# Performance work log

Measured on AMD Instinct MI355X. Metric: run time of the kernel, lower is better.

Reference implementation:

```python
import jax, jax.numpy as jnp
import numpy as np

B, T, I, H, L = 128, 512, 512, 1024, 2
KEEP = 0.9  # 1 - dropout_rate


def setup_inputs() -> dict:
    key = jax.random.key(0)
    ks = jax.random.split(key, 13)
    s = 0.02
    bern = lambda k, shape: (jax.random.bernoulli(k, KEEP, shape) / KEEP).astype(jnp.float32)
    return {
        "x": jax.random.normal(ks[0], (B, T, I), dtype=jnp.float32),
        "W_ih0": jax.random.normal(ks[1], (4 * H, I), dtype=jnp.float32) * s,
        "W_hh0": jax.random.normal(ks[2], (4 * H, H), dtype=jnp.float32) * s,
        "b_ih0": jax.random.normal(ks[3], (4 * H,), dtype=jnp.float32) * s,
        "b_hh0": jax.random.normal(ks[4], (4 * H,), dtype=jnp.float32) * s,
        "W_ih1": jax.random.normal(ks[5], (4 * H, H), dtype=jnp.float32) * s,
        "W_hh1": jax.random.normal(ks[6], (4 * H, H), dtype=jnp.float32) * s,
        "b_ih1": jax.random.normal(ks[7], (4 * H,), dtype=jnp.float32) * s,
        "b_hh1": jax.random.normal(ks[8], (4 * H,), dtype=jnp.float32) * s,
        "out_mask": bern(ks[9], (L, B, H)),
        "h_mask": bern(ks[10], (L, B, H)),
        "c_mask": bern(ks[11], (L, B, H)),
    }


def _run_layer(x_tbi, W_ih, W_hh, b_ih, b_hh, om, hm, cm):
    """x_tbi: [T,B,in]; masks: [B,H]. Returns ([T,B,H] outputs, final (h,c))."""
    h0 = jnp.zeros((x_tbi.shape[1], H), dtype=x_tbi.dtype)
    c0 = jnp.zeros_like(h0)
    # precompute input projections for all timesteps: [T,B,4H]
    xg = jnp.einsum('tbi,gi->tbg', x_tbi, W_ih) + b_ih + b_hh

    def step(carry, xg_t):
        h, c = carry
        gates = xg_t + h @ W_hh.T  # [B,4H]
        i, f, g, o = jnp.split(gates, 4, axis=-1)
        i, f, o = jax.nn.sigmoid(i), jax.nn.sigmoid(f), jax.nn.sigmoid(o)
        g = jnp.tanh(g)
        c2 = f * c + i * g
        h2 = o * jnp.tanh(c2)
        out = h2 * om
        return (h2 * hm, c2 * cm), out

    (hf, cf), ys = jax.lax.scan(step, (h0, c0), xg)
    return ys, (hf, cf)


def reference(x, W_ih0, W_hh0, b_ih0, b_hh0, W_ih1, W_hh1, b_ih1, b_hh1,
              out_mask, h_mask, c_mask):
    layers = [(W_ih0, W_hh0, b_ih0, b_hh0), (W_ih1, W_hh1, b_ih1, b_hh1)]
    xt = jnp.transpose(x, (1, 0, 2))  # [T,B,I]
    for l, (Wi, Wh, bi, bh) in enumerate(layers):
        xt, (hf, cf) = _run_layer(xt, Wi, Wh, bi, bh,
                                  out_mask[l], h_mask[l], c_mask[l])
    out = jnp.transpose(xt, (1, 0, 2))  # [B,T,H]
    return out, (hf[None], cf[None])
```

## Files before the change

kernel.cpp:

```cpp
#include <hip/hip_runtime.h>

#define B_  128
#define T_  512
#define I_  512
#define H_  1024
#define G4  4096
#define SLOT 262144L
#define SENTW 0xFFFFFFFFu

typedef __attribute__((ext_vector_type(8))) short   short8;
typedef __attribute__((ext_vector_type(4))) short   short4v;
typedef __attribute__((ext_vector_type(4))) float   f32x4;
typedef unsigned long long u64;

__device__ __forceinline__ float bf2f(short u){
  return __uint_as_float(((unsigned)(unsigned short)u) << 16);
}
__device__ __forceinline__ short f2bf(float f){
  unsigned u = __float_as_uint(f);
  unsigned r = (u + 0x7FFFu + ((u >> 16) & 1u)) >> 16;
  return (short)r;
}
__device__ __forceinline__ float sigm(float x){ return 1.0f/(1.0f + __expf(-x)); }
__device__ __forceinline__ float tanh_(float x){ return 1.0f - 2.0f/(__expf(2.0f*x) + 1.0f); }
__device__ __forceinline__ bool okq(u64 a){
  return ((unsigned)a != SENTW) & ((unsigned)(a >> 32) != SENTW);
}

__global__ __launch_bounds__(256) void cvt_bf16(const float* __restrict__ in,
                                                short* __restrict__ out, int nq){
  int i = blockIdx.x*256 + threadIdx.x;
  if (i >= nq) return;
  float4 v = ((const float4*)in)[i];
  short4v o; o.x = f2bf(v.x); o.y = f2bf(v.y); o.z = f2bf(v.z); o.w = f2bf(v.w);
  ((short4v*)out)[i] = o;
}

__global__ __launch_bounds__(256) void swz_whh(const float* __restrict__ W,
                                               short* __restrict__ out){
  int c = blockIdx.x*256 + threadIdx.x;
  int l = c & 63, ks = (c >> 6) & 15, ct = (c >> 10) & 1, wvv = (c >> 11) & 7, jb = c >> 14;
  int g = wvv >> 1, kh = wvv & 1;
  long row = (long)(g*1024 + jb*32 + ct*16 + (l & 15));
  int col = kh*512 + ks*32 + (l >> 4)*8;
  const float* src = W + row*H_ + col;
  short8 o;
#pragma unroll
  for (int e = 0; e < 8; ++e) o[e] = f2bf(src[e]);
  ((short8*)out)[c] = o;
}

template<int K>
__global__ __launch_bounds__(256) void proj_gemm(const short* __restrict__ A,
                                                 const short* __restrict__ W,
                                                 const float* __restrict__ bih,
                                                 const float* __restrict__ bhh,
                                                 short* __restrict__ C){
  __shared__ short lds[2][2][128*40];
  const int tid = threadIdx.x;
  const int l  = tid & 63, wv = tid >> 6;
  const int wm = wv >> 1,  wn = wv & 1;
  const int nt = blockIdx.x, mt = blockIdx.y;
  const int r0 = tid >> 2, cb = (tid & 3) * 8;
  const short* Ab = A + (long)(mt*128 + r0)*K + cb;
  const short* Wb = W + (long)(nt*128 + r0)*K + cb;
  const int lo  = r0*40 + cb;
  const int lo2 = lo + 64*40;
  const int NK = K/32;

  short8 pa0 = *(const short8*)(Ab);
  short8 pa1 = *(const short8*)(Ab + 64*K);
  short8 pb0 = *(const short8*)(Wb);
  short8 pb1 = *(const short8*)(Wb + 64*K);
  *(short8*)&lds[0][0][lo]  = pa0;
  *(short8*)&lds[0][0][lo2] = pa1;
  *(short8*)&lds[0][1][lo]  = pb0;
  *(short8*)&lds[0][1][lo2] = pb1;

  f32x4 acc[4][4];
  f32x4 z = {0.f,0.f,0.f,0.f};
#pragma unroll
  for (int i = 0; i < 4; ++i)
#pragma unroll
    for (int j = 0; j < 4; ++j) acc[i][j] = z;

  for (int kt = 0; kt < NK; ++kt){
    __syncthreads();
    if (kt + 1 < NK){
      pa0 = *(const short8*)(Ab + (kt+1)*32);
      pa1 = *(const short8*)(Ab + (kt+1)*32 + 64*K);
      pb0 = *(const short8*)(Wb + (kt+1)*32);
      pb1 = *(const short8*)(Wb + (kt+1)*32 + 64*K);
    }
    const short* As = lds[kt & 1][0];
    const short* Bs = lds[kt & 1][1];
    short8 bfr[4];
#pragma unroll
    for (int nf = 0; nf < 4; ++nf)
      bfr[nf] = *(const short8*)&Bs[(wn*64 + nf*16 + (l & 15))*40 + (l >> 4)*8];
#pragma unroll
    for (int mf = 0; mf < 4; ++mf){
      short8 af = *(const short8*)&As[(wm*64 + mf*16 + (l & 15))*40 + (l >> 4)*8];
#pragma unroll
      for (int nf = 0; nf < 4; ++nf)
        acc[mf][nf] = __builtin_amdgcn_mfma_f32_16x16x32_bf16(af, bfr[nf], acc[mf][nf], 0, 0, 0);
    }
    if (kt + 1 < NK){
      int nb = (kt + 1) & 1;
      *(short8*)&lds[nb][0][lo]  = pa0;
      *(short8*)&lds[nb][0][lo2] = pa1;
      *(short8*)&lds[nb][1][lo]  = pb0;
      *(short8*)&lds[nb][1][lo2] = pb1;
    }
  }

  const int mrow0 = mt*128 + wm*64;
  const int ncol0 = nt*128 + wn*64;
#pragma unroll
  for (int nf = 0; nf < 4; ++nf){
    int n = ncol0 + nf*16 + (l & 15);
    int g   = n >> 10;
    int jb  = (n & 1023) >> 5;
    int jl5 = n & 31;
    float bs = bih[n] + bhh[n];
#pragma unroll
    for (int mf = 0; mf < 4; ++mf){
#pragma unroll
      for (int r = 0; r < 4; ++r){
        int m = mrow0 + mf*16 + (l >> 4)*4 + r;
        int b = m >> 9, t = m & 511;
        int idx2 = (jl5 >> 3)*16 + (b & 15);
        int pos  = (idx2 >> 3)*64 + (idx2 & 7)*8 + (jl5 & 7);
        long o = ((((long)t*8 + (b >> 4))*32 + jb)*4 + g)*512 + pos;
        C[o] = f2bf(acc[mf][nf][r] + bs);
      }
    }
  }
}

template<int LAYER, bool RING>
__global__ __launch_bounds__(512, 2) void lstm_scan(
    short* __restrict__ hring,
    const short* __restrict__ Wsw, const short* __restrict__ xg,
    const float* __restrict__ om, const float* __restrict__ hm, const float* __restrict__ cm,
    short* __restrict__ out0, float* __restrict__ dout,
    int* __restrict__ flags)
{
  const int tid = threadIdx.x;
  const int l = tid & 63, wv = tid >> 6;
  const int bt = blockIdx.x, jb = blockIdx.y;

  short8 w0[16], w1[16];
  {
    const short8* wp = (const short8*)Wsw + ((long)((jb*8 + wv)*2)*16)*64 + l;
#pragma unroll
    for (int ks = 0; ks < 16; ++ks) w0[ks] = wp[ks*64];
#pragma unroll
    for (int ks = 0; ks < 16; ++ks) w1[ks] = wp[(16 + ks)*64];
    f32x4* wf0 = (f32x4*)w0;
    f32x4* wf1 = (f32x4*)w1;
#pragma unroll
    for (int i = 0; i < 16; ++i){ asm volatile("" : "+v"(wf0[i])); asm volatile("" : "+v"(wf1[i])); }
  }

  const int idx = wv*8 + (l >> 3);
  const int bl  = idx & 15;
  const int jl  = ((idx >> 4) << 3) + (l & 7);
  const int jcol = jb*32 + jl;
  const long bj = (long)(bt*16 + bl)*H_ + jcol;
  const float mo = om[bj], mh = hm[bj], mc = cm[bj];
  float c = 0.f;
  const int ct_r = jl >> 4;
  const int lane_src = (jl & 15) + ((bl >> 2) << 4);
  const int rr = bl & 3;
  const int kh = wv & 1;

  __shared__ __align__(16) short hbuf[2048*8];
  __shared__ float red[16*264];
  __shared__ __align__(16) short sstage[512];
  int* flbase = flags + (long)bt*T_*32;

  const long go0 = (long)(wv*256 + 0*64 + l)*2;
  const long go1 = (long)(wv*256 + 1*64 + l)*2;
  const long go2 = (long)(wv*256 + 2*64 + l)*2;
  const long go3 = (long)(wv*256 + 3*64 + l)*2;

  const short* xg0 = xg + (((long)bt)*32 + jb)*2048;
  short xv0 = xg0[tid], xv1 = xg0[512 + tid], xv2 = xg0[1024 + tid], xv3 = xg0[1536 + tid];

  for (int t = 0; t < T_; ++t){
    const long slotoff  = RING ? (long)t*SLOT     : (long)(t & 1)*SLOT;
    const long nslotoff = RING ? (long)(t+1)*SLOT : (long)((t+1) & 1)*SLOT;

    if (t > 0){
      const u64* hp = (const u64*)((const char*)hring + slotoff + (long)bt*32768);
      if constexpr (RING){
        u64 q0=0,q1=0,q2=0,q3=0,q4=0,q5=0,q6=0,q7=0;
        int ok = 0, spins = 0;
        while (true){
          if (!(ok & 1)){
            u64 a = __hip_atomic_load(hp + go0,     __ATOMIC_RELAXED, __HIP_MEMORY_SCOPE_AGENT);
            u64 b = __hip_atomic_load(hp + go0 + 1, __ATOMIC_RELAXED, __HIP_MEMORY_SCOPE_AGENT);
            if (okq(a) & okq(b)){ q0 = a; q1 = b; ok |= 1; }
          }
          if (!(ok & 2)){
            u64 a = __hip_atomic_load(hp + go1,     __ATOMIC_RELAXED, __HIP_MEMORY_SCOPE_AGENT);
            u64 b = __hip_atomic_load(hp + go1 + 1, __ATOMIC_RELAXED, __HIP_MEMORY_SCOPE_AGENT);
            if (okq(a) & okq(b)){ q2 = a; q3 = b; ok |= 2; }
          }
          if (!(ok & 4)){
            u64 a = __hip_atomic_load(hp + go2,     __ATOMIC_RELAXED, __HIP_MEMORY_SCOPE_AGENT);
            u64 b = __hip_atomic_load(hp + go2 + 1, __ATOMIC_RELAXED, __HIP_MEMORY_SCOPE_AGENT);
            if (okq(a) & okq(b)){ q4 = a; q5 = b; ok |= 4; }
          }
          if (!(ok & 8)){
            u64 a = __hip_atomic_load(hp + go3,     __ATOMIC_RELAXED, __HIP_MEMORY_SCOPE_AGENT);
            u64 b = __hip_atomic_load(hp + go3 + 1, __ATOMIC_RELAXED, __HIP_MEMORY_SCOPE_AGENT);
            if (okq(a) & okq(b)){ q6 = a; q7 = b; ok |= 8; }
          }
          if (ok == 15) break;
          if (++spins > (1 << 20)) break;
          if (spins > 2) __builtin_amdgcn_s_sleep(2);
        }
        union { u64 u[2]; short8 s; } c0, c1, c2_, c3;
        c0.u[0] = q0; c0.u[1] = q1;  c1.u[0] = q2; c1.u[1] = q3;
        c2_.u[0] = q4; c2_.u[1] = q5; c3.u[0] = q6; c3.u[1] = q7;
        *(short8*)&hbuf[(wv*256 +   0 + l)*8] = c0.s;
        *(short8*)&hbuf[(wv*256 +  64 + l)*8] = c1.s;
        *(short8*)&hbuf[(wv*256 + 128 + l)*8] = c2_.s;
        *(short8*)&hbuf[(wv*256 + 192 + l)*8] = c3.s;
      } else {
        short8 vv[4];
#pragma unroll
        for (int i = 0; i < 4; ++i){
          const u64* ap = hp + (long)(wv*256 + i*64 + l)*2;
          union { u64 q[2]; short8 s; } uu;
          uu.q[0] = __hip_atomic_load(ap,     __ATOMIC_RELAXED, __HIP_MEMORY_SCOPE_AGENT);
          uu.q[1] = __hip_atomic_load(ap + 1, __ATOMIC_RELAXED, __HIP_MEMORY_SCOPE_AGENT);
          vv[i] = uu.s;
        }
#pragma unroll
        for (int i = 0; i < 4; ++i)
          *(short8*)&hbuf[(wv*256 + i*64 + l)*8] = vv[i];
      }
      __syncthreads();

      f32x4 a00 = {0.f,0.f,0.f,0.f}, a01 = {0.f,0.f,0.f,0.f};
      f32x4 a10 = {0.f,0.f,0.f,0.f}, a11 = {0.f,0.f,0.f,0.f};
#pragma unroll
      for (int ks = 0; ks < 16; ++ks){
        short8 av = *(const short8*)&hbuf[((kh*16 + ks)*64 + l)*8];
        if (ks & 1){
          a01 = __builtin_amdgcn_mfma_f32_16x16x32_bf16(av, w0[ks], a01, 0, 0, 0);
          a11 = __builtin_amdgcn_mfma_f32_16x16x32_bf16(av, w1[ks], a11, 0, 0, 0);
        } else {
          a00 = __builtin_amdgcn_mfma_f32_16x16x32_bf16(av, w0[ks], a00, 0, 0, 0);
          a10 = __builtin_amdgcn_mfma_f32_16x16x32_bf16(av, w1[ks], a10, 0, 0, 0);
        }
      }
      f32x4 s0, s1;
#pragma unroll
      for (int r = 0; r < 4; ++r){ s0[r] = a00[r] + a01[r]; s1[r] = a10[r] + a11[r]; }
      *(f32x4*)&red[(wv*2 + 0)*264 + l*4] = s0;
      *(f32x4*)&red[(wv*2 + 1)*264 + l*4] = s1;
      __syncthreads();
    }

    float gate[4];
    short xvv[4] = {xv0, xv1, xv2, xv3};
#pragma unroll
    for (int g = 0; g < 4; ++g){
      float rv = 0.f;
      if (t > 0){
        rv = red[((g*2 + 0)*2 + ct_r)*264 + lane_src*4 + rr]
           + red[((g*2 + 1)*2 + ct_r)*264 + lane_src*4 + rr];
      }
      gate[g] = rv + bf2f(xvv[g]);
    }
    float ii = sigm(gate[0]);
    float ff = sigm(gate[1]);
    float gg = tanh_(gate[2]);
    float oo = sigm(gate[3]);
    float c2 = ff*c + ii*gg;
    float h2 = oo*tanh_(c2);
    c = c2*mc;
    float hn = h2*mh;

    if (t == T_ - 1){
      if (LAYER == 0){
        out0[((long)(bt*16 + bl)*T_ + t)*H_ + jcol] = f2bf(h2*mo);
      } else {
        dout[((long)(bt*16 + bl)*T_ + t)*H_ + jcol] = h2*mo;
        dout[(long)B_*T_*H_ + bj] = hn;
        dout[(long)B_*T_*H_ + (long)B_*H_ + bj] = c;
      }
      break;
    }

    sstage[wv*64 + l] = f2bf(hn);
    asm volatile("s_waitcnt lgkmcnt(0)" ::: "memory");
    __builtin_amdgcn_sched_barrier(0);
    if (l < 8){
      short8 pk = *(const short8*)&sstage[wv*64 + l*8];
      char* hdst = (char*)hring + nslotoff
                 + ((long)bt*2048 + jb*64 + wv*8 + l)*16;
      if constexpr (RING){
        asm volatile("global_store_dwordx4 %0, %1, off sc1" :: "v"(hdst), "v"(pk) : "memory");
      } else {
        union { short8 s; u64 q[2]; } uu; uu.s = pk;
        u64* qp = (u64*)hdst;
        __hip_atomic_store(qp,     uu.q[0], __ATOMIC_RELAXED, __HIP_MEMORY_SCOPE_AGENT);
        __hip_atomic_store(qp + 1, uu.q[1], __ATOMIC_RELAXED, __HIP_MEMORY_SCOPE_AGENT);
      }
    }
    if constexpr (!RING){
      asm volatile("s_waitcnt vmcnt(0)" ::: "memory");
      __syncthreads();
      if (tid == 0)
        __hip_atomic_store(&flbase[(long)t*32 + jb], 1,
                           __ATOMIC_RELAXED, __HIP_MEMORY_SCOPE_AGENT);
    }

    if (LAYER == 0){
      out0[((long)(bt*16 + bl)*T_ + t)*H_ + jcol] = f2bf(h2*mo);
    } else {
      dout[((long)(bt*16 + bl)*T_ + t)*H_ + jcol] = h2*mo;
    }
    const short* xgn = xg + (((long)(t+1)*8 + bt)*32 + jb)*2048;
    xv0 = xgn[tid]; xv1 = xgn[512 + tid]; xv2 = xgn[1024 + tid]; xv3 = xgn[1536 + tid];

    if constexpr (!RING){
      const u64* fp = (const u64*)&flbase[(long)t*32];
      int spins = 0;
      while (true){
        int ok = 1;
        if (l < 16){
          u64 v = __hip_atomic_load(fp + l, __ATOMIC_RELAXED, __HIP_MEMORY_SCOPE_AGENT);
          ok = ((unsigned)v != 0u) & ((unsigned)(v >> 32) != 0u);
        }
        if (__all(ok)) break;
        if (++spins > (1 << 20)) break;
        if (spins > 8) __builtin_amdgcn_s_sleep(1);
      }
      __builtin_amdgcn_sched_barrier(0);
      __builtin_amdgcn_fence(__ATOMIC_ACQUIRE, "workgroup");
    }
  }
}

extern "C" void kernel_launch(void* const* d_in, const int* in_sizes, int n_in,
                              void* d_out, int out_size, void* d_ws, size_t ws_size,
                              hipStream_t stream){
  const float* x    = (const float*)d_in[0];
  const float* Wih0 = (const float*)d_in[1];
  const float* Whh0 = (const float*)d_in[2];
  const float* bih0 = (const float*)d_in[3];
  const float* bhh0 = (const float*)d_in[4];
  const float* Wih1 = (const float*)d_in[5];
  const float* Whh1 = (const float*)d_in[6];
  const float* bih1 = (const float*)d_in[7];
  const float* bhh1 = (const float*)d_in[8];
  const float* omsk = (const float*)d_in[9];
  const float* hmsk = (const float*)d_in[10];
  const float* cmsk = (const float*)d_in[11];
  float* out = (float*)d_out;

  char* p = (char*)d_ws;
  auto alloc = [&](size_t bytes)->char*{
    char* r = p; p += (bytes + 255) & ~(size_t)255; return r;
  };
  short* xg      = (short*)alloc((size_t)65536*4096*2);
  short* out0_bf = (short*)alloc((size_t)67108864*2);
  short* x_bf    = (short*)out0_bf;
  short* wih0_bf = (short*)alloc((size_t)2097152*2);
  short* wih1_bf = (short*)alloc((size_t)4194304*2);
  short* whh0_sw = (short*)alloc((size_t)4194304*2);
  short* whh1_sw = (short*)alloc((size_t)4194304*2);
  int*   flags0  = (int*)alloc((size_t)8*512*32*4);
  int*   flags1  = (int*)alloc((size_t)8*512*32*4);
  size_t fixed = (size_t)(p - (char*)d_ws);
  bool ring = (fixed + (size_t)512*SLOT) <= ws_size;
  size_t ringbytes = ring ? (size_t)512*SLOT : (size_t)2*SLOT;
  short* hring = (short*)alloc(ringbytes);
  if ((size_t)(p - (char*)d_ws) > ws_size) return;

  hipMemsetAsync(flags0, 0, (size_t)8*512*32*4, stream);
  hipMemsetAsync(flags1, 0, (size_t)8*512*32*4, stream);
  hipMemsetAsync(hring, 0xFF, ringbytes, stream);

  cvt_bf16<<<33554432/4/256, 256, 0, stream>>>(x,    x_bf,    33554432/4);
  cvt_bf16<<<2097152/4/256,  256, 0, stream>>>(Wih0, wih0_bf, 2097152/4);
  cvt_bf16<<<4194304/4/256,  256, 0, stream>>>(Wih1, wih1_bf, 4194304/4);
  swz_whh <<<524288/256,     256, 0, stream>>>(Whh0, whh0_sw);
  swz_whh <<<524288/256,     256, 0, stream>>>(Whh1, whh1_sw);

  proj_gemm<512><<<dim3(32, 512), 256, 0, stream>>>(x_bf, wih0_bf, bih0, bhh0, xg);
  if (ring)
    lstm_scan<0, true ><<<dim3(8, 32), 512, 0, stream>>>(hring, whh0_sw, xg,
        omsk, hmsk, cmsk, out0_bf, nullptr, flags0);
  else
    lstm_scan<0, false><<<dim3(8, 32), 512, 0, stream>>>(hring, whh0_sw, xg,
        omsk, hmsk, cmsk, out0_bf, nullptr, flags0);

  hipMemsetAsync(hring, 0xFF, ringbytes, stream);

  proj_gemm<1024><<<dim3(32, 512), 256, 0, stream>>>(out0_bf, wih1_bf, bih1, bhh1, xg);
  if (ring)
    lstm_scan<1, true ><<<dim3(8, 32), 512, 0, stream>>>(hring, whh1_sw, xg,
        omsk + 131072, hmsk + 131072, cmsk + 131072, nullptr, out, flags1);
  else
    lstm_scan<1, false><<<dim3(8, 32), 512, 0, stream>>>(hring, whh1_sw, xg,
        omsk + 131072, hmsk + 131072, cmsk + 131072, nullptr, out, flags1);
}
```

Baseline: 4.577 ms.

## Store input projections row-major via LDS-staged coalesced writes, read directly in scan

The projection GEMM epilogue now stages the bf16 results in shared memory and writes them as contiguous 16-byte vectors into a plain row-major [B*T,4H] buffer. Previously each element went out as a separate 2-byte store into a swizzled per-step tile layout. The scan kernel now indexes that row-major buffer by batch row, time and gate column. This is meant to cut the cost of the scattered GEMM output stores. In exchange, the per-step xg prefetch in the scan is less contiguous than before, since it was previously one packed 4 KB tile per block.

```diff
diff --git a/kernel.cpp b/kernel.cpp
--- a/kernel.cpp
+++ b/kernel.cpp
@@ -56,7 +56,7 @@
                                                  const float* __restrict__ bih,
                                                  const float* __restrict__ bhh,
                                                  short* __restrict__ C){
-  __shared__ short lds[2][2][128*40];
+  __shared__ __align__(16) short lds[2][2][128*40];
   const int tid = threadIdx.x;
   const int l  = tid & 63, wv = tid >> 6;
   const int wm = wv >> 1,  wn = wv & 1;
@@ -114,27 +114,30 @@
     }
   }
 
-  const int mrow0 = mt*128 + wm*64;
-  const int ncol0 = nt*128 + wn*64;
+  __syncthreads();
+  short* cst = (short*)&lds[0][0][0];
 #pragma unroll
   for (int nf = 0; nf < 4; ++nf){
-    int n = ncol0 + nf*16 + (l & 15);
-    int g   = n >> 10;
-    int jb  = (n & 1023) >> 5;
-    int jl5 = n & 31;
+    int nc = wn*64 + nf*16 + (l & 15);
+    int n  = nt*128 + nc;
     float bs = bih[n] + bhh[n];
 #pragma unroll
     for (int mf = 0; mf < 4; ++mf){
 #pragma unroll
       for (int r = 0; r < 4; ++r){
-        int m = mrow0 + mf*16 + (l >> 4)*4 + r;
-        int b = m >> 9, t = m & 511;
-        int idx2 = (jl5 >> 3)*16 + (b & 15);
-        int pos  = (idx2 >> 3)*64 + (idx2 & 7)*8 + (jl5 & 7);
-        long o = ((((long)t*8 + (b >> 4))*32 + jb)*4 + g)*512 + pos;
-        C[o] = f2bf(acc[mf][nf][r] + bs);
-      }
-    }
+        int mr = wm*64 + mf*16 + (l >> 4)*4 + r;
+        cst[mr*132 + nc] = f2bf(acc[mf][nf][r] + bs);
+      }
+    }
+  }
+  __syncthreads();
+  const long m0 = (long)mt*128;
+  const int  n0 = nt*128;
+#pragma unroll
+  for (int i = 0; i < 8; ++i){
+    int sid = i*256 + tid;
+    int mr = sid >> 4, seg = sid & 15;
+    *(short8*)&C[(m0 + mr)*G4 + n0 + seg*8] = *(const short8*)&cst[mr*132 + seg*8];
   }
 }
 
@@ -185,8 +188,8 @@
   const long go2 = (long)(wv*256 + 2*64 + l)*2;
   const long go3 = (long)(wv*256 + 3*64 + l)*2;
 
-  const short* xg0 = xg + (((long)bt)*32 + jb)*2048;
-  short xv0 = xg0[tid], xv1 = xg0[512 + tid], xv2 = xg0[1024 + tid], xv3 = xg0[1536 + tid];
+  const long xbase = (long)(bt*16 + bl)*T_*G4 + jcol;
+  short xv0 = xg[xbase], xv1 = xg[xbase + H_], xv2 = xg[xbase + 2*H_], xv3 = xg[xbase + 3*H_];
 
   for (int t = 0; t < T_; ++t){
     const long slotoff  = RING ? (long)t*SLOT     : (long)(t & 1)*SLOT;
@@ -326,8 +329,10 @@
     } else {
       dout[((long)(bt*16 + bl)*T_ + t)*H_ + jcol] = h2*mo;
     }
-    const short* xgn = xg + (((long)(t+1)*8 + bt)*32 + jb)*2048;
-    xv0 = xgn[tid]; xv1 = xgn[512 + tid]; xv2 = xgn[1024 + tid]; xv3 = xgn[1536 + tid];
+    {
+      const short* xp = xg + xbase + (long)(t + 1)*G4;
+      xv0 = xp[0]; xv1 = xp[H_]; xv2 = xp[2*H_]; xv3 = xp[3*H_];
+    }
 
     if constexpr (!RING){
       const u64* fp = (const u64*)&flbase[(long)t*32];
```

New measurement: 4.101 ms. 1.12x faster.
